# Optimization experiments

Measured on AMD Instinct MI355X. Metric: run time of the kernel, lower is better.

The kernel has to match this reference:

```python
import jax, jax.numpy as jnp
import numpy as np

FFT_LEN = 512
HOP = 256
WIN_LEN = 1024


def setup_inputs() -> dict:
    key = jax.random.key(0)
    k1, k2 = jax.random.split(key)
    inputs = jax.random.normal(k1, (8, 514, 4000), dtype=jnp.float32)
    win = jax.random.uniform(k2, (WIN_LEN,), dtype=jnp.float32)
    return {"inputs": inputs, "win": win}


def reference(inputs, win):
    B, D, T = inputs.shape  # D == 514
    half = FFT_LEN // 2  # 256
    real = inputs[:, :half, :]            # [B,256,T]
    imag = inputs[:, half + 1:-1, :]      # [B,256,T]
    c = jax.lax.complex(real, imag)       # bins 0..255
    # conjugate-symmetric extension: bin 256 = 0, bins 257..511 = conj(bins 255..1)
    tail = jnp.conj(jnp.flip(c[:, 1:, :], axis=1))            # [B,255,T]
    zero = jnp.zeros_like(c[:, :1, :])
    spec = jnp.concatenate([c, zero, tail], axis=1)           # [B,512,T]
    # torch does fft over the freq axis and keeps the real part
    ifft_data = jnp.real(jnp.fft.fft(spec, axis=1)).astype(jnp.float32)  # [B,512,T]
    tmp = jnp.concatenate([ifft_data, ifft_data], axis=1)     # [B,1024,T]
    tmp = tmp * win[None, :, None] * 256.0
    # overlap-add via four shifted padded copies (faithful to the original)
    t1 = jnp.pad(tmp, ((0, 0), (0, 768), (0, 3)))
    t2 = jnp.pad(tmp, ((0, 0), (256, 512), (1, 2)))
    t3 = jnp.pad(tmp, ((0, 0), (512, 256), (2, 1)))
    t4 = jnp.pad(tmp, ((0, 0), (768, 0), (3, 0)))
    synbuf = t1 + t2 + t3 + t4                                # [B,1792,T+3]
    syn = synbuf[:, 768:1024, :-4]                            # [B,256,T-1]
    syn = jnp.flip(syn, axis=1)
    syn = jnp.transpose(syn, (0, 2, 1)).reshape(B, -1)        # [B,256*(T-1)]
    return syn
```

## Files before the change

### kernel.cpp

```cpp
#include <hip/hip_runtime.h>


typedef __attribute__((ext_vector_type(8))) short short8;
typedef __attribute__((ext_vector_type(8))) __bf16 bf16x8;
typedef __attribute__((ext_vector_type(4))) float floatx4;
typedef __attribute__((ext_vector_type(4))) unsigned uintx4;

__device__ inline unsigned bfbits(float f) {
  unsigned u = __builtin_bit_cast(unsigned, f);
  return (u + 0x7fffu + ((u >> 16) & 1u)) >> 16;
}

__device__ inline short f2bf(float f) { return (short)(unsigned short)bfbits(f); }

__device__ inline unsigned pk2bf(float a, float b) {
  return (bfbits(a) & 0xffffu) | (bfbits(b) << 16);
}

#define PI_OVER_256 0.01227184630308513f

__global__ void build_m(short* __restrict__ M) {
  int idx = blockIdx.x * blockDim.x + threadIdx.x;
  int ntile = idx >> 10;
  int s = (idx >> 6) & 15;
  int lane = idx & 63;
  int n = ntile * 16 + (lane & 15);
  int kb = lane >> 4;
  short8 v;
#pragma unroll
  for (int e = 0; e < 8; e++) {
    int kap = s * 32 + kb * 8 + e;
    int gk = 2 * (kap & 255) + (kap >> 8);
    float val;
    if (gk == 0) {
      val = 1.0f;
    } else if (gk < 256) {
      int m = (n * gk) & 511;
      val = 2.0f * __cosf((float)m * PI_OVER_256);
    } else {
      int m = (n * (gk - 256)) & 511;
      val = 2.0f * __sinf((float)m * PI_OVER_256);
    }
    v[e] = f2bf(val);
  }
  ((short8*)M)[idx] = v;
}

__device__ inline int lds_off(int col, int g) {
  return col * 512 + (((g & 56) | ((g + col) & 7)) << 3);
}

__global__ __launch_bounds__(512, 4) void gemm_ola(
    const float* __restrict__ in, const float* __restrict__ win,
    const short* __restrict__ M, float* __restrict__ out) {
  __shared__ short ldsX[32 * 512];

  const int tid = threadIdx.x;
  const int bid = blockIdx.x;
  const int b = bid & 7;
  const int tile = bid >> 3;
  const int c0 = 28 * tile - 4;

  {
    const int cbase = 4 * (tid & 7);
    const int gg = tid >> 3;
    const int kap0 = gg * 8;
    const int gc = c0 + cbase;
    floatx4 f[8];
    if (gc >= 0 && gc <= 3996) {
      const float* src = in + (size_t)b * 2056000 + gc;
#pragma unroll
      for (int j = 0; j < 8; j++) {
        int kap = kap0 + j;
        int gk = 2 * (kap & 255) + (kap >> 8);
        int row = (gk < 256) ? gk : gk + 1;
        f[j] = *(const floatx4*)(src + (size_t)row * 4000);
      }
    } else {
#pragma unroll
      for (int j = 0; j < 8; j++) f[j] = floatx4{0.f, 0.f, 0.f, 0.f};
    }
#pragma unroll
    for (int cc = 0; cc < 4; cc++) {
      const int col = cbase + cc;
      uintx4 u;
#pragma unroll
      for (int i = 0; i < 4; i++) u[i] = pk2bf(f[2 * i][cc], f[2 * i + 1][cc]);
      *(uintx4*)&ldsX[lds_off(col, gg)] = u;
    }
  }
  __syncthreads();

  const int w = tid >> 6;
  const int lane = tid & 63;
  const int c = lane & 15;
  const int kb = lane >> 4;
  const int rg = kb;

  floatx4 accE[2][2] = {};
  floatx4 accO[2][2] = {};

  const short8* Mf = (const short8*)M;
  const int J0 = 2 * w, J1 = 2 * w + 1;

  bf16x8 c00 = __builtin_bit_cast(bf16x8, Mf[(J0 * 16 + 0) * 64 + lane]);
  bf16x8 c01 = __builtin_bit_cast(bf16x8, Mf[(J1 * 16 + 0) * 64 + lane]);
  bf16x8 n00 = __builtin_bit_cast(bf16x8, Mf[(J0 * 16 + 1) * 64 + lane]);
  bf16x8 n01 = __builtin_bit_cast(bf16x8, Mf[(J1 * 16 + 1) * 64 + lane]);
  bf16x8 a0 = __builtin_bit_cast(bf16x8, *(const short8*)&ldsX[lds_off(c, kb)]);
  bf16x8 a1 = __builtin_bit_cast(bf16x8, *(const short8*)&ldsX[lds_off(16 + c, kb)]);

#pragma unroll
  for (int s = 0; s < 16; s++) {
    bf16x8 f00, f01, na0, na1;
    if (s < 14) {
      f00 = __builtin_bit_cast(bf16x8, Mf[(J0 * 16 + s + 2) * 64 + lane]);
      f01 = __builtin_bit_cast(bf16x8, Mf[(J1 * 16 + s + 2) * 64 + lane]);
    }
    if (s < 15) {
      const int g = 4 * (s + 1) + kb;
      na0 = __builtin_bit_cast(bf16x8, *(const short8*)&ldsX[lds_off(c, g)]);
      na1 = __builtin_bit_cast(bf16x8, *(const short8*)&ldsX[lds_off(16 + c, g)]);
    }
    if (s < 8) {
      accE[0][0] = __builtin_amdgcn_mfma_f32_16x16x32_bf16(a0, c00, accE[0][0], 0, 0, 0);
      accE[0][1] = __builtin_amdgcn_mfma_f32_16x16x32_bf16(a0, c01, accE[0][1], 0, 0, 0);
      accE[1][0] = __builtin_amdgcn_mfma_f32_16x16x32_bf16(a1, c00, accE[1][0], 0, 0, 0);
      accE[1][1] = __builtin_amdgcn_mfma_f32_16x16x32_bf16(a1, c01, accE[1][1], 0, 0, 0);
    } else {
      accO[0][0] = __builtin_amdgcn_mfma_f32_16x16x32_bf16(a0, c00, accO[0][0], 0, 0, 0);
      accO[0][1] = __builtin_amdgcn_mfma_f32_16x16x32_bf16(a0, c01, accO[0][1], 0, 0, 0);
      accO[1][0] = __builtin_amdgcn_mfma_f32_16x16x32_bf16(a1, c00, accO[1][0], 0, 0, 0);
      accO[1][1] = __builtin_amdgcn_mfma_f32_16x16x32_bf16(a1, c01, accO[1][1], 0, 0, 0);
    }
    c00 = n00; c01 = n01; n00 = f00; n01 = f01;
    a0 = na0; a1 = na1;
  }

#pragma unroll
  for (int jt = 0; jt < 2; jt++) {
    const int J = 2 * w + jt;
    const int j = 16 * J + c;
    const float wv0 = 256.0f * win[768 + j];
    const float wv1 = 256.0f * win[512 + j];
    const float wv2 = 256.0f * win[256 + j];
    const float wv3 = 256.0f * win[j];

    floatx4 Y[2], Yh[2];
#pragma unroll
    for (int q = 0; q < 2; q++) {
      Y[q] = accE[q][jt] + accO[q][jt];
      Yh[q] = accE[q][jt] - accO[q][jt];
    }

#pragma unroll
    for (int q = 0; q < 2; q++) {
      const int qm = (q > 0) ? q - 1 : 0;
      float yb[4], yhb[4];
#pragma unroll
      for (int p = 1; p < 4; p++) {
        float z = (rg == 3) ? Y[qm][p] : Y[q][p];
        yb[p] = __shfl(z, lane + 48, 64);
      }
#pragma unroll
      for (int p = 2; p < 4; p++) {
        float z = (rg == 3) ? Yh[qm][p] : Yh[q][p];
        yhb[p] = __shfl(z, lane + 48, 64);
      }
      floatx4 v;
#pragma unroll
      for (int p = 0; p < 4; p++) {
        float t1 = (p >= 1) ? Y[q][p - 1] : yb[3];
        float t2 = (p >= 2) ? Yh[q][p - 2] : yhb[p + 2];
        float t3 = (p >= 3) ? Y[q][p - 3] : yb[p + 1];
        v[p] = wv0 * Yh[q][p] + wv1 * t1 + wv2 * t2 + wv3 * t3;
      }
#pragma unroll
      for (int p = 0; p < 4; p++) {
        const int L = 16 * q + 4 * rg + p;
        const int t = c0 + L;
        if (L >= 4 && t <= 3998) {
          out[((size_t)b * 3999 + t) * 256 + (255 - j)] = v[p];
        }
      }
    }
  }
}

extern "C" void kernel_launch(void* const* d_in, const int* in_sizes, int n_in,
                              void* d_out, int out_size, void* d_ws, size_t ws_size,
                              hipStream_t stream) {
  const float* in = (const float*)d_in[0];
  const float* win = (const float*)d_in[1];
  float* out = (float*)d_out;
  short* M = (short*)d_ws;

  hipLaunchKernelGGL(build_m, dim3(64), dim3(256), 0, stream, M);
  hipLaunchKernelGGL(gemm_ola, dim3(1144), dim3(512), 0, stream, in, win, M, out);
}
```

Baseline: 121.0 us.

## Process two column tiles per block with double-buffered LDS prefetch

Each block now handles two consecutive 28-column tiles, halving the grid. The global loads for the second tile are issued before the first tile's MFMA loop and written into a second LDS buffer afterwards, so load latency overlaps compute. This doubles LDS use to 64KB per block and raises register pressure from the held prefetch registers, which can lower occupancy. It also leaves fewer blocks to spread across CUs.

```diff
diff --git a/kernel.cpp b/kernel.cpp
--- a/kernel.cpp
+++ b/kernel.cpp
@@ -53,22 +53,25 @@
 __global__ __launch_bounds__(512, 4) void gemm_ola(
     const float* __restrict__ in, const float* __restrict__ win,
     const short* __restrict__ M, float* __restrict__ out) {
-  __shared__ short ldsX[32 * 512];
+  __shared__ short ldsX[2][32 * 512];
 
   const int tid = threadIdx.x;
   const int bid = blockIdx.x;
   const int b = bid & 7;
-  const int tile = bid >> 3;
-  const int c0 = 28 * tile - 4;
-
-  {
-    const int cbase = 4 * (tid & 7);
-    const int gg = tid >> 3;
-    const int kap0 = gg * 8;
+  const int pair = bid >> 3;
+  const int c0_0 = 56 * pair - 4;
+
+  const int cbase = 4 * (tid & 7);
+  const int gg = tid >> 3;
+  const int kap0 = gg * 8;
+  const float* srcb = in + (size_t)b * 2056000;
+
+  floatx4 f[8];
+
+  auto issue_loads = [&](int c0) {
     const int gc = c0 + cbase;
-    floatx4 f[8];
     if (gc >= 0 && gc <= 3996) {
-      const float* src = in + (size_t)b * 2056000 + gc;
+      const float* src = srcb + gc;
 #pragma unroll
       for (int j = 0; j < 8; j++) {
         int kap = kap0 + j;
@@ -80,15 +83,20 @@
 #pragma unroll
       for (int j = 0; j < 8; j++) f[j] = floatx4{0.f, 0.f, 0.f, 0.f};
     }
+  };
+  auto write_lds = [&](int buf) {
 #pragma unroll
     for (int cc = 0; cc < 4; cc++) {
       const int col = cbase + cc;
       uintx4 u;
 #pragma unroll
       for (int i = 0; i < 4; i++) u[i] = pk2bf(f[2 * i][cc], f[2 * i + 1][cc]);
-      *(uintx4*)&ldsX[lds_off(col, gg)] = u;
-    }
-  }
+      *(uintx4*)&ldsX[buf][lds_off(col, gg)] = u;
+    }
+  };
+
+  issue_loads(c0_0);
+  write_lds(0);
   __syncthreads();
 
   const int w = tid >> 6;
@@ -96,94 +104,105 @@
   const int c = lane & 15;
   const int kb = lane >> 4;
   const int rg = kb;
-
-  floatx4 accE[2][2] = {};
-  floatx4 accO[2][2] = {};
-
   const short8* Mf = (const short8*)M;
   const int J0 = 2 * w, J1 = 2 * w + 1;
 
-  bf16x8 c00 = __builtin_bit_cast(bf16x8, Mf[(J0 * 16 + 0) * 64 + lane]);
-  bf16x8 c01 = __builtin_bit_cast(bf16x8, Mf[(J1 * 16 + 0) * 64 + lane]);
-  bf16x8 n00 = __builtin_bit_cast(bf16x8, Mf[(J0 * 16 + 1) * 64 + lane]);
-  bf16x8 n01 = __builtin_bit_cast(bf16x8, Mf[(J1 * 16 + 1) * 64 + lane]);
-  bf16x8 a0 = __builtin_bit_cast(bf16x8, *(const short8*)&ldsX[lds_off(c, kb)]);
-  bf16x8 a1 = __builtin_bit_cast(bf16x8, *(const short8*)&ldsX[lds_off(16 + c, kb)]);
-
-#pragma unroll
-  for (int s = 0; s < 16; s++) {
-    bf16x8 f00, f01, na0, na1;
-    if (s < 14) {
-      f00 = __builtin_bit_cast(bf16x8, Mf[(J0 * 16 + s + 2) * 64 + lane]);
-      f01 = __builtin_bit_cast(bf16x8, Mf[(J1 * 16 + s + 2) * 64 + lane]);
-    }
-    if (s < 15) {
-      const int g = 4 * (s + 1) + kb;
-      na0 = __builtin_bit_cast(bf16x8, *(const short8*)&ldsX[lds_off(c, g)]);
-      na1 = __builtin_bit_cast(bf16x8, *(const short8*)&ldsX[lds_off(16 + c, g)]);
-    }
-    if (s < 8) {
-      accE[0][0] = __builtin_amdgcn_mfma_f32_16x16x32_bf16(a0, c00, accE[0][0], 0, 0, 0);
-      accE[0][1] = __builtin_amdgcn_mfma_f32_16x16x32_bf16(a0, c01, accE[0][1], 0, 0, 0);
-      accE[1][0] = __builtin_amdgcn_mfma_f32_16x16x32_bf16(a1, c00, accE[1][0], 0, 0, 0);
-      accE[1][1] = __builtin_amdgcn_mfma_f32_16x16x32_bf16(a1, c01, accE[1][1], 0, 0, 0);
-    } else {
-      accO[0][0] = __builtin_amdgcn_mfma_f32_16x16x32_bf16(a0, c00, accO[0][0], 0, 0, 0);
-      accO[0][1] = __builtin_amdgcn_mfma_f32_16x16x32_bf16(a0, c01, accO[0][1], 0, 0, 0);
-      accO[1][0] = __builtin_amdgcn_mfma_f32_16x16x32_bf16(a1, c00, accO[1][0], 0, 0, 0);
-      accO[1][1] = __builtin_amdgcn_mfma_f32_16x16x32_bf16(a1, c01, accO[1][1], 0, 0, 0);
-    }
-    c00 = n00; c01 = n01; n00 = f00; n01 = f01;
-    a0 = na0; a1 = na1;
-  }
-
-#pragma unroll
-  for (int jt = 0; jt < 2; jt++) {
-    const int J = 2 * w + jt;
-    const int j = 16 * J + c;
-    const float wv0 = 256.0f * win[768 + j];
-    const float wv1 = 256.0f * win[512 + j];
-    const float wv2 = 256.0f * win[256 + j];
-    const float wv3 = 256.0f * win[j];
-
-    floatx4 Y[2], Yh[2];
-#pragma unroll
-    for (int q = 0; q < 2; q++) {
-      Y[q] = accE[q][jt] + accO[q][jt];
-      Yh[q] = accE[q][jt] - accO[q][jt];
-    }
-
-#pragma unroll
-    for (int q = 0; q < 2; q++) {
-      const int qm = (q > 0) ? q - 1 : 0;
-      float yb[4], yhb[4];
-#pragma unroll
-      for (int p = 1; p < 4; p++) {
-        float z = (rg == 3) ? Y[qm][p] : Y[q][p];
-        yb[p] = __shfl(z, lane + 48, 64);
-      }
-#pragma unroll
-      for (int p = 2; p < 4; p++) {
-        float z = (rg == 3) ? Yh[qm][p] : Yh[q][p];
-        yhb[p] = __shfl(z, lane + 48, 64);
-      }
-      floatx4 v;
-#pragma unroll
-      for (int p = 0; p < 4; p++) {
-        float t1 = (p >= 1) ? Y[q][p - 1] : yb[3];
-        float t2 = (p >= 2) ? Yh[q][p - 2] : yhb[p + 2];
-        float t3 = (p >= 3) ? Y[q][p - 3] : yb[p + 1];
-        v[p] = wv0 * Yh[q][p] + wv1 * t1 + wv2 * t2 + wv3 * t3;
-      }
-#pragma unroll
-      for (int p = 0; p < 4; p++) {
-        const int L = 16 * q + 4 * rg + p;
-        const int t = c0 + L;
-        if (L >= 4 && t <= 3998) {
-          out[((size_t)b * 3999 + t) * 256 + (255 - j)] = v[p];
-        }
-      }
-    }
+#pragma unroll
+  for (int half = 0; half < 2; half++) {
+    const int c0 = c0_0 + 28 * half;
+    const short* Xb = ldsX[half];
+
+    if (half == 0) issue_loads(c0_0 + 28);
+
+    floatx4 accE[2][2] = {};
+    floatx4 accO[2][2] = {};
+
+    bf16x8 c00 = __builtin_bit_cast(bf16x8, Mf[(J0 * 16 + 0) * 64 + lane]);
+    bf16x8 c01 = __builtin_bit_cast(bf16x8, Mf[(J1 * 16 + 0) * 64 + lane]);
+    bf16x8 n00 = __builtin_bit_cast(bf16x8, Mf[(J0 * 16 + 1) * 64 + lane]);
+    bf16x8 n01 = __builtin_bit_cast(bf16x8, Mf[(J1 * 16 + 1) * 64 + lane]);
+    bf16x8 a0 = __builtin_bit_cast(bf16x8, *(const short8*)&Xb[lds_off(c, kb)]);
+    bf16x8 a1 = __builtin_bit_cast(bf16x8, *(const short8*)&Xb[lds_off(16 + c, kb)]);
+
+#pragma unroll
+    for (int s = 0; s < 16; s++) {
+      bf16x8 f00, f01, na0, na1;
+      if (s < 14) {
+        f00 = __builtin_bit_cast(bf16x8, Mf[(J0 * 16 + s + 2) * 64 + lane]);
+        f01 = __builtin_bit_cast(bf16x8, Mf[(J1 * 16 + s + 2) * 64 + lane]);
+      }
+      if (s < 15) {
+        const int g = 4 * (s + 1) + kb;
+        na0 = __builtin_bit_cast(bf16x8, *(const short8*)&Xb[lds_off(c, g)]);
+        na1 = __builtin_bit_cast(bf16x8, *(const short8*)&Xb[lds_off(16 + c, g)]);
+      }
+      if (s < 8) {
+        accE[0][0] = __builtin_amdgcn_mfma_f32_16x16x32_bf16(a0, c00, accE[0][0], 0, 0, 0);
+        accE[0][1] = __builtin_amdgcn_mfma_f32_16x16x32_bf16(a0, c01, accE[0][1], 0, 0, 0);
+        accE[1][0] = __builtin_amdgcn_mfma_f32_16x16x32_bf16(a1, c00, accE[1][0], 0, 0, 0);
+        accE[1][1] = __builtin_amdgcn_mfma_f32_16x16x32_bf16(a1, c01, accE[1][1], 0, 0, 0);
+      } else {
+        accO[0][0] = __builtin_amdgcn_mfma_f32_16x16x32_bf16(a0, c00, accO[0][0], 0, 0, 0);
+        accO[0][1] = __builtin_amdgcn_mfma_f32_16x16x32_bf16(a0, c01, accO[0][1], 0, 0, 0);
+        accO[1][0] = __builtin_amdgcn_mfma_f32_16x16x32_bf16(a1, c00, accO[1][0], 0, 0, 0);
+        accO[1][1] = __builtin_amdgcn_mfma_f32_16x16x32_bf16(a1, c01, accO[1][1], 0, 0, 0);
+      }
+      c00 = n00; c01 = n01; n00 = f00; n01 = f01;
+      a0 = na0; a1 = na1;
+    }
+
+    if (half == 0) write_lds(1);
+
+#pragma unroll
+    for (int jt = 0; jt < 2; jt++) {
+      const int J = 2 * w + jt;
+      const int j = 16 * J + c;
+      const float wv0 = 256.0f * win[768 + j];
+      const float wv1 = 256.0f * win[512 + j];
+      const float wv2 = 256.0f * win[256 + j];
+      const float wv3 = 256.0f * win[j];
+
+      floatx4 Y[2], Yh[2];
+#pragma unroll
+      for (int q = 0; q < 2; q++) {
+        Y[q] = accE[q][jt] + accO[q][jt];
+        Yh[q] = accE[q][jt] - accO[q][jt];
+      }
+
+#pragma unroll
+      for (int q = 0; q < 2; q++) {
+        const int qm = (q > 0) ? q - 1 : 0;
+        float yb[4], yhb[4];
+#pragma unroll
+        for (int p = 1; p < 4; p++) {
+          float z = (rg == 3) ? Y[qm][p] : Y[q][p];
+          yb[p] = __shfl(z, lane + 48, 64);
+        }
+#pragma unroll
+        for (int p = 2; p < 4; p++) {
+          float z = (rg == 3) ? Yh[qm][p] : Yh[q][p];
+          yhb[p] = __shfl(z, lane + 48, 64);
+        }
+        floatx4 v;
+#pragma unroll
+        for (int p = 0; p < 4; p++) {
+          float t1 = (p >= 1) ? Y[q][p - 1] : yb[3];
+          float t2 = (p >= 2) ? Yh[q][p - 2] : yhb[p + 2];
+          float t3 = (p >= 3) ? Y[q][p - 3] : yb[p + 1];
+          v[p] = wv0 * Yh[q][p] + wv1 * t1 + wv2 * t2 + wv3 * t3;
+        }
+#pragma unroll
+        for (int p = 0; p < 4; p++) {
+          const int L = 16 * q + 4 * rg + p;
+          const int t = c0 + L;
+          if (L >= 4 && t <= 3998) {
+            out[((size_t)b * 3999 + t) * 256 + (255 - j)] = v[p];
+          }
+        }
+      }
+    }
+
+    if (half == 0) __syncthreads();
   }
 }
 
@@ -196,5 +215,5 @@
   short* M = (short*)d_ws;
 
   hipLaunchKernelGGL(build_m, dim3(64), dim3(256), 0, stream, M);
-  hipLaunchKernelGGL(gemm_ola, dim3(1144), dim3(512), 0, stream, in, win, M, out);
-}
+  hipLaunchKernelGGL(gemm_ola, dim3(576), dim3(512), 0, stream, in, win, M, out);
+}
```

After: 124.1 us. 2.6% more time.
